# Performance work log

Hardware: AMD Instinct MI355X
Metric: run time of the kernel (lower is better)

## Reference

```python
import jax, jax.numpy as jnp
import numpy as np

B, N, H, O = 4096, 32, 64, 32  # batch, input_dim, hidden_dim, output_dim


def setup_inputs() -> dict:
    key = jax.random.key(0)
    ks = jax.random.split(key, 9)
    s = 0.1
    return {
        "x": jax.random.normal(ks[0], (B, N), jnp.float32),
        "phi_w1": jax.random.normal(ks[1], (H, 1), jnp.float32) * s,
        "phi_b1": jax.random.normal(ks[2], (H,), jnp.float32) * s,
        "phi_w2": jax.random.normal(ks[3], (O, H), jnp.float32) * s,
        "phi_b2": jax.random.normal(ks[4], (O,), jnp.float32) * s,
        "psi_w1": jax.random.normal(ks[5], (H, 2 * O), jnp.float32) * s,
        "psi_b1": jax.random.normal(ks[6], (H,), jnp.float32) * s,
        "psi_w2": jax.random.normal(ks[7], (O, H), jnp.float32) * s,
        "psi_b2": jax.random.normal(ks[8], (O,), jnp.float32) * s,
    }


def reference(x, phi_w1, phi_b1, phi_w2, phi_b2, psi_w1, psi_b1, psi_w2, psi_b2):
    n = x.shape[1]
    # phi applied per scalar column, batched: [B, N, H]
    h1 = jax.nn.relu(x[..., None] * phi_w1[:, 0] + phi_b1)
    phi_out = jnp.einsum('bnh,oh->bno', h1, phi_w2) + phi_b2  # [B, N, O]
    # all i<j pairs (static indices)
    ii, jj = np.triu_indices(n, k=1)  # P = n*(n-1)/2
    pairs = jnp.concatenate([phi_out[:, ii], phi_out[:, jj]], axis=-1)  # [B, P, 2O]
    h2 = jax.nn.relu(jnp.einsum('bpt,ht->bph', pairs, psi_w1) + psi_b1)  # [B, P, H]
    psi_out = jnp.einsum('bph,oh->bpo', h2, psi_w2) + psi_b2  # [B, P, O]
    return jnp.sum(psi_out, axis=1)  # [B, O]
```

## Files before the change

kernel.cpp:

```cpp
#include <hip/hip_runtime.h>

namespace {

typedef float v2f  __attribute__((ext_vector_type(2)));
typedef float v4f  __attribute__((ext_vector_type(4)));
typedef float f32x16 __attribute__((ext_vector_type(16)));
typedef short bf16x8 __attribute__((ext_vector_type(8)));
typedef unsigned short ushort;
typedef unsigned short us8 __attribute__((ext_vector_type(8)));

constexpr int NDIM = 32;
constexpr int HDIM = 64;
constexpr int ODIM = 32;
constexpr float PAIRS = 496.0f;

__device__ __forceinline__ ushort f2bf(float f) {
    unsigned int u = __builtin_bit_cast(unsigned int, f);
    u += 0x7fffu + ((u >> 16) & 1u);
    return (ushort)(u >> 16);
}

__global__ __launch_bounds__(64) void kan_precompute(
    const float* __restrict__ phi_w2, const float* __restrict__ phi_b2,
    const float* __restrict__ psi_w1, const float* __restrict__ psi_b1,
    ushort* __restrict__ Bfrag, float* __restrict__ cconst)
{
    const int s = blockIdx.x >> 2, c = blockIdx.x & 3;
    const int lane = threadIdx.x;
    const int row = lane & 31, half = lane >> 5;
    const int hh = 32 * c + row;
    const int h = hh & 63;
    const int off = (hh >= 64) ? ODIM : 0;

    us8 out8;
#pragma unroll
    for (int e = 0; e < 8; ++e) {
        const int k = 16 * s + 8 * half + e;
        float m = 0.f;
#pragma unroll
        for (int o = 0; o < ODIM; ++o)
            m = fmaf(psi_w1[h * 2 * ODIM + off + o], phi_w2[o * HDIM + k], m);
        out8[e] = f2bf(m);
    }
    *(us8*)(Bfrag + (size_t)(blockIdx.x * 64 + lane) * 8) = out8;

    if (blockIdx.x == 0) {
        float cch = psi_b1[lane];
#pragma unroll
        for (int o = 0; o < ODIM; ++o)
            cch = fmaf(psi_w1[lane * 2 * ODIM + o] + psi_w1[lane * 2 * ODIM + ODIM + o],
                       phi_b2[o], cch);
        cconst[lane] = cch;
    }
}

__global__ __launch_bounds__(256, 4) void kan_main(
    const float* __restrict__ x, const float* __restrict__ phi_w1,
    const float* __restrict__ phi_b1, const float* __restrict__ psi_w2,
    const float* __restrict__ psi_b2, const ushort* __restrict__ Bfrag,
    const float* __restrict__ cconst, float* __restrict__ out)
{
    __shared__ float sred[4][HDIM];

    const int tid  = threadIdx.x;
    const int wave = tid >> 6;
    const int lane = tid & 63;
    const int batch = blockIdx.x * 4 + wave;
    const int row  = lane & 31;
    const int half = lane >> 5;
    const bool hi  = lane >= 32;

    const float xn = x[(size_t)batch * NDIM + row];
    bf16x8 afrag[4];
#pragma unroll
    for (int s = 0; s < 4; ++s) {
        const int kb = 16 * s + 8 * half;
        const v4f w1a = *(const v4f*)(phi_w1 + kb);
        const v4f w1b = *(const v4f*)(phi_w1 + kb + 4);
        const v4f b1a = *(const v4f*)(phi_b1 + kb);
        const v4f b1b = *(const v4f*)(phi_b1 + kb + 4);
        bf16x8 t;
#pragma unroll
        for (int e = 0; e < 4; ++e)
            t[e] = (short)f2bf(fmaxf(fmaf(xn, w1a[e], b1a[e]), 0.f));
#pragma unroll
        for (int e = 0; e < 4; ++e)
            t[4 + e] = (short)f2bf(fmaxf(fmaf(xn, w1b[e], b1b[e]), 0.f));
        afrag[s] = t;
    }

    const float cc0 = cconst[row];
    const float cc1 = cconst[32 + row];
    f32x16 acc0, acc1, acc2, acc3;
#pragma unroll
    for (int r = 0; r < 16; ++r) { acc0[r] = cc0; acc1[r] = cc1; acc2[r] = 0.f; acc3[r] = 0.f; }

    const bf16x8* Bf = (const bf16x8*)Bfrag;
#pragma unroll
    for (int s = 0; s < 4; ++s) {
        const bf16x8 b0 = Bf[(s * 4 + 0) * 64 + lane];
        const bf16x8 b1 = Bf[(s * 4 + 1) * 64 + lane];
        const bf16x8 b2 = Bf[(s * 4 + 2) * 64 + lane];
        const bf16x8 b3 = Bf[(s * 4 + 3) * 64 + lane];
        acc0 = __builtin_amdgcn_mfma_f32_32x32x16_bf16(afrag[s], b0, acc0, 0, 0, 0);
        acc1 = __builtin_amdgcn_mfma_f32_32x32x16_bf16(afrag[s], b1, acc1, 0, 0, 0);
        acc2 = __builtin_amdgcn_mfma_f32_32x32x16_bf16(afrag[s], b2, acc2, 0, 0, 0);
        acc3 = __builtin_amdgcn_mfma_f32_32x32x16_bf16(afrag[s], b3, acc3, 0, 0, 0);
    }

    v2f Ap0[8], Ap1[8], Bp0[8], Bp1[8];
#pragma unroll
    for (int q = 0; q < 8; ++q) {
        v2f own, snd, oth;
        own.x = hi ? acc1[2 * q]     : acc0[2 * q];
        own.y = hi ? acc1[2 * q + 1] : acc0[2 * q + 1];
        snd.x = hi ? acc0[2 * q]     : acc1[2 * q];
        snd.y = hi ? acc0[2 * q + 1] : acc1[2 * q + 1];
        oth.x = __shfl_xor(snd.x, 32);
        oth.y = __shfl_xor(snd.y, 32);
        Ap0[q].x = hi ? oth.x : own.x;  Ap0[q].y = hi ? oth.y : own.y;
        Ap1[q].x = hi ? own.x : oth.x;  Ap1[q].y = hi ? own.y : oth.y;
    }
#pragma unroll
    for (int q = 0; q < 8; ++q) {
        v2f own, snd, oth;
        own.x = hi ? acc3[2 * q]     : acc2[2 * q];
        own.y = hi ? acc3[2 * q + 1] : acc2[2 * q + 1];
        snd.x = hi ? acc2[2 * q]     : acc3[2 * q];
        snd.y = hi ? acc2[2 * q + 1] : acc3[2 * q + 1];
        oth.x = __shfl_xor(snd.x, 32);
        oth.y = __shfl_xor(snd.y, 32);
        Bp0[q].x = hi ? oth.x : own.x;  Bp0[q].y = hi ? oth.y : own.y;
        Bp1[q].x = hi ? own.x : oth.x;  Bp1[q].y = hi ? own.y : oth.y;
    }

    auto AF = [&](int n) -> float {
        const v2f p = ((n >> 2) & 1) ? Ap1[(n >> 3) * 2 + ((n & 3) >> 1)]
                                     : Ap0[(n >> 3) * 2 + ((n & 3) >> 1)];
        return (n & 1) ? p.y : p.x;
    };
    auto BPair = [&](int p) -> v2f {
        return ((p >> 1) & 1) ? Bp1[(p >> 2) * 2 + (p & 1)]
                              : Bp0[(p >> 2) * 2 + (p & 1)];
    };
    auto BFs = [&](int n) -> float {
        const v2f p = BPair(n >> 1);
        return (n & 1) ? p.y : p.x;
    };

    v2f vacc0 = {0.f, 0.f}, vacc1 = {0.f, 0.f};
    float sacc = 0.f;
#pragma unroll
    for (int i = 0; i < NDIM - 1; ++i) {
        const float ai = AF(i);
        int j = i + 1;
        if (j & 1) { sacc += fmaxf(ai + BFs(j), 0.f); ++j; }
        const v2f ai2 = {ai, ai};
#pragma unroll
        for (int p = j >> 1; p < 16; ++p) {
            const v2f t = ai2 + BPair(p);
            v2f m;
            m.x = fmaxf(t.x, 0.f);
            m.y = fmaxf(t.y, 0.f);
            if (p & 1) vacc1 += m; else vacc0 += m;
        }
    }
    const float S = sacc + (vacc0.x + vacc0.y) + (vacc1.x + vacc1.y);

    sred[wave][lane] = S;
    __builtin_amdgcn_s_waitcnt(0);

    const int oo = row;
    const float* w2r = psi_w2 + (size_t)oo * HDIM + half * 32;
    float part = 0.f;
#pragma unroll
    for (int r = 0; r < 8; ++r) {
        const v4f w = *(const v4f*)(w2r + 4 * r);
        const float* sr = &sred[wave][half * 32 + 4 * r];
        part = fmaf(w[0], sr[0], part);
        part = fmaf(w[1], sr[1], part);
        part = fmaf(w[2], sr[2], part);
        part = fmaf(w[3], sr[3], part);
    }
    part += __shfl_down(part, 32);
    if (!hi)
        out[(size_t)batch * ODIM + oo] = part + PAIRS * psi_b2[oo];
}

}

extern "C" void kernel_launch(void* const* d_in, const int* in_sizes, int n_in,
                              void* d_out, int out_size, void* d_ws, size_t ws_size,
                              hipStream_t stream)
{
    const float* x      = (const float*)d_in[0];
    const float* phi_w1 = (const float*)d_in[1];
    const float* phi_b1 = (const float*)d_in[2];
    const float* phi_w2 = (const float*)d_in[3];
    const float* phi_b2 = (const float*)d_in[4];
    const float* psi_w1 = (const float*)d_in[5];
    const float* psi_b1 = (const float*)d_in[6];
    const float* psi_w2 = (const float*)d_in[7];
    const float* psi_b2 = (const float*)d_in[8];

    ushort* Bfrag = (ushort*)d_ws;
    float* cconst = (float*)((char*)d_ws + 16 * 64 * 8 * sizeof(ushort));
    float* out    = (float*)d_out;

    kan_precompute<<<16, 64, 0, stream>>>(phi_w2, phi_b2, psi_w1, psi_b1, Bfrag, cconst);
    kan_main<<<4096 / 4, 256, 0, stream>>>(x, phi_w1, phi_b1, psi_w2, psi_b2,
                                           Bfrag, cconst, out);
}
```

Measured before the change: 23.12 us.

## Use packed fp16 pair-ReLU sums, stage B fragments in LDS, tile precompute in shared

The O(N^2) pair ReLU accumulation now runs in packed half precision, using pk_add, pk_max and fdot2 to sum two pairs per instruction, where it previously used fp32 pair-vector ops. B fragments are loaded cooperatively into LDS once per block rather than each wave reading them from global memory, and the precompute kernel stages its weights in shared memory. The fp16 rounding (round-toward-zero conversion) reduces accuracy of the pairwise sums, and the added __syncthreads adds a block barrier.

Result: faster. 22.18 us (-4.1%).

```diff
diff --git a/kernel.cpp b/kernel.cpp
--- a/kernel.cpp
+++ b/kernel.cpp
@@ -8,6 +8,8 @@
 typedef short bf16x8 __attribute__((ext_vector_type(8)));
 typedef unsigned short ushort;
 typedef unsigned short us8 __attribute__((ext_vector_type(8)));
+typedef unsigned int v4u __attribute__((ext_vector_type(4)));
+typedef __fp16 h2 __attribute__((ext_vector_type(2)));
 
 constexpr int NDIM = 32;
 constexpr int HDIM = 64;
@@ -25,12 +27,31 @@
     const float* __restrict__ psi_w1, const float* __restrict__ psi_b1,
     ushort* __restrict__ Bfrag, float* __restrict__ cconst)
 {
+    __shared__ float pw2s[32 * 64];
+    __shared__ float pw1s[32 * 36];
+
     const int s = blockIdx.x >> 2, c = blockIdx.x & 3;
     const int lane = threadIdx.x;
+    const int hbase = (c & 1) * 32;
+    const int off   = (c >> 1) * ODIM;
+
+#pragma unroll
+    for (int it = 0; it < 8; ++it) {
+        const int idx = it * 256 + lane * 4;
+        *(v4f*)&pw2s[idx] = *(const v4f*)(phi_w2 + idx);
+    }
+#pragma unroll
+    for (int it = 0; it < 16; ++it) {
+        const int idx = it * 64 + lane;
+        const int r = idx >> 5, col = idx & 31;
+        pw1s[r * 36 + col] = psi_w1[(hbase + r) * 2 * ODIM + off + col];
+    }
+    __syncthreads();
+
     const int row = lane & 31, half = lane >> 5;
-    const int hh = 32 * c + row;
-    const int h = hh & 63;
-    const int off = (hh >= 64) ? ODIM : 0;
+    v4f w1r[8];
+#pragma unroll
+    for (int t = 0; t < 8; ++t) w1r[t] = *(const v4f*)&pw1s[row * 36 + 4 * t];
 
     us8 out8;
 #pragma unroll
@@ -38,8 +59,8 @@
         const int k = 16 * s + 8 * half + e;
         float m = 0.f;
 #pragma unroll
-        for (int o = 0; o < ODIM; ++o)
-            m = fmaf(psi_w1[h * 2 * ODIM + off + o], phi_w2[o * HDIM + k], m);
+        for (int o = 0; o < 32; ++o)
+            m = fmaf(w1r[o >> 2][o & 3], pw2s[o * 64 + k], m);
         out8[e] = f2bf(m);
     }
     *(us8*)(Bfrag + (size_t)(blockIdx.x * 64 + lane) * 8) = out8;
@@ -60,6 +81,7 @@
     const float* __restrict__ psi_b2, const ushort* __restrict__ Bfrag,
     const float* __restrict__ cconst, float* __restrict__ out)
 {
+    __shared__ v4u  Blds[1024];
     __shared__ float sred[4][HDIM];
 
     const int tid  = threadIdx.x;
@@ -70,7 +92,14 @@
     const int half = lane >> 5;
     const bool hi  = lane >= 32;
 
+    const v4u* gB = (const v4u*)Bfrag;
+    const v4u t0 = gB[tid];
+    const v4u t1 = gB[tid + 256];
+    const v4u t2 = gB[tid + 512];
+    const v4u t3 = gB[tid + 768];
+
     const float xn = x[(size_t)batch * NDIM + row];
+
     bf16x8 afrag[4];
 #pragma unroll
     for (int s = 0; s < 4; ++s) {
@@ -91,11 +120,18 @@
 
     const float cc0 = cconst[row];
     const float cc1 = cconst[32 + row];
+
+    Blds[tid]       = t0;
+    Blds[tid + 256] = t1;
+    Blds[tid + 512] = t2;
+    Blds[tid + 768] = t3;
+    __syncthreads();
+
     f32x16 acc0, acc1, acc2, acc3;
 #pragma unroll
     for (int r = 0; r < 16; ++r) { acc0[r] = cc0; acc1[r] = cc1; acc2[r] = 0.f; acc3[r] = 0.f; }
 
-    const bf16x8* Bf = (const bf16x8*)Bfrag;
+    const bf16x8* Bf = (const bf16x8*)Blds;
 #pragma unroll
     for (int s = 0; s < 4; ++s) {
         const bf16x8 b0 = Bf[(s * 4 + 0) * 64 + lane];
@@ -134,56 +170,60 @@
         Bp1[q].x = hi ? own.x : oth.x;  Bp1[q].y = hi ? own.y : oth.y;
     }
 
-    auto AF = [&](int n) -> float {
-        const v2f p = ((n >> 2) & 1) ? Ap1[(n >> 3) * 2 + ((n & 3) >> 1)]
-                                     : Ap0[(n >> 3) * 2 + ((n & 3) >> 1)];
-        return (n & 1) ? p.y : p.x;
-    };
-    auto BPair = [&](int p) -> v2f {
-        return ((p >> 1) & 1) ? Bp1[(p >> 2) * 2 + (p & 1)]
-                              : Bp0[(p >> 2) * 2 + (p & 1)];
-    };
-    auto BFs = [&](int n) -> float {
-        const v2f p = BPair(n >> 1);
-        return (n & 1) ? p.y : p.x;
-    };
-
-    v2f vacc0 = {0.f, 0.f}, vacc1 = {0.f, 0.f};
-    float sacc = 0.f;
-#pragma unroll
-    for (int i = 0; i < NDIM - 1; ++i) {
-        const float ai = AF(i);
-        int j = i + 1;
-        if (j & 1) { sacc += fmaxf(ai + BFs(j), 0.f); ++j; }
-        const v2f ai2 = {ai, ai};
-#pragma unroll
-        for (int p = j >> 1; p < 16; ++p) {
-            const v2f t = ai2 + BPair(p);
-            v2f m;
-            m.x = fmaxf(t.x, 0.f);
-            m.y = fmaxf(t.y, 0.f);
-            if (p & 1) vacc1 += m; else vacc0 += m;
+    float Af[NDIM], Bn[NDIM];
+#pragma unroll
+    for (int q = 0; q < 8; ++q) {
+        const int n0 = ((2 * q) & 3) + 8 * ((2 * q) >> 2);
+        Af[n0]     = Ap0[q].x;  Af[n0 + 1] = Ap0[q].y;
+        Af[n0 + 4] = Ap1[q].x;  Af[n0 + 5] = Ap1[q].y;
+        Bn[n0]     = Bp0[q].x;  Bn[n0 + 1] = Bp0[q].y;
+        Bn[n0 + 4] = Bp1[q].x;  Bn[n0 + 5] = Bp1[q].y;
+    }
+
+    h2 Bh[16];
+#pragma unroll
+    for (int p = 0; p < 16; ++p)
+        Bh[p] = __builtin_amdgcn_cvt_pkrtz(Bn[2 * p], Bn[2 * p + 1]);
+
+    const h2 one2  = {(__fp16)1.f, (__fp16)1.f};
+    const h2 zero2 = {(__fp16)0.f, (__fp16)0.f};
+    float acc[8] = {0.f, 0.f, 0.f, 0.f, 0.f, 0.f, 0.f, 0.f};
+
+#pragma unroll
+    for (int t = 0; t < 8; ++t) {
+        const h2 ae = __builtin_amdgcn_cvt_pkrtz(Af[4 * t],     Af[4 * t + 2]);
+        const h2 bo = __builtin_amdgcn_cvt_pkrtz(Bn[4 * t + 1], Bn[4 * t + 3]);
+        const h2 m  = __builtin_elementwise_max(ae + bo, zero2);
+        acc[t] = __builtin_amdgcn_fdot2(m, one2, acc[t], false);
+    }
+#pragma unroll
+    for (int i = 0; i < 30; ++i) {
+        const h2 ai2 = __builtin_amdgcn_cvt_pkrtz(Af[i], Af[i]);
+#pragma unroll
+        for (int p = i / 2 + 1; p < 16; ++p) {
+            const h2 m = __builtin_elementwise_max(ai2 + Bh[p], zero2);
+            acc[p & 7] = __builtin_amdgcn_fdot2(m, one2, acc[p & 7], false);
         }
     }
-    const float S = sacc + (vacc0.x + vacc0.y) + (vacc1.x + vacc1.y);
+    const float S = ((acc[0] + acc[1]) + (acc[2] + acc[3])) +
+                    ((acc[4] + acc[5]) + (acc[6] + acc[7]));
 
     sred[wave][lane] = S;
-    __builtin_amdgcn_s_waitcnt(0);
 
     const int oo = row;
     const float* w2r = psi_w2 + (size_t)oo * HDIM + half * 32;
     float part = 0.f;
 #pragma unroll
     for (int r = 0; r < 8; ++r) {
-        const v4f w = *(const v4f*)(w2r + 4 * r);
-        const float* sr = &sred[wave][half * 32 + 4 * r];
-        part = fmaf(w[0], sr[0], part);
-        part = fmaf(w[1], sr[1], part);
-        part = fmaf(w[2], sr[2], part);
-        part = fmaf(w[3], sr[3], part);
+        const v4f w  = *(const v4f*)(w2r + 4 * r);
+        const v4f sv = *(const v4f*)&sred[wave][half * 32 + 4 * r];
+        part = fmaf(w[0], sv[0], part);
+        part = fmaf(w[1], sv[1], part);
+        part = fmaf(w[2], sv[2], part);
+        part = fmaf(w[3], sv[3], part);
     }
     part += __shfl_down(part, 32);
-    if (!hi)
+    if (half == 0)
         out[(size_t)batch * ODIM + oo] = part + PAIRS * psi_b2[oo];
 }
 
```
